# Kernel tuning notes

Hardware: AMD Instinct MI355X
Metric: run time of the kernel (lower is better)

## Reference

```python
import jax, jax.numpy as jnp
import numpy as np

N, T, D, E1 = 64, 32, 128, 128
EPS = 1e-6


def _mlp(x, W1, b1, W2, b2):
    # Linear -> ReLU -> (Dropout: identity in eval) -> Linear
    return jnp.maximum(x @ W1 + b1, 0.0) @ W2 + b2


def _forward(x_time, x_news,
             it_W1, it_b1, it_W2, it_b2,
             inw_W1, inw_b1, inw_W2, inw_b2,
             t2n_W1, t2n_b1, t2n_W2, t2n_b2,
             n2t_W1, n2t_b1, n2t_W2, n2t_b2,
             f_W1, f_b1, f_W2, f_b2,
             theta_t, theta_n):
    xt = x_time.reshape(-1, D)   # [NT, D]
    xn = x_news.reshape(-1, D)   # [NT, D]

    # incidence-matrix candidates, each [NT, E1]
    H_time = xt @ _mlp(xt.T, it_W1, it_b1, it_W2, it_b2)
    H_news = xn @ _mlp(xn.T, inw_W1, inw_b1, inw_W2, inw_b2)
    H_t2n = xt @ _mlp(xn.T, t2n_W1, t2n_b1, t2n_W2, t2n_b2)
    H_n2t = xn @ _mlp(xt.T, n2t_W1, n2t_b1, n2t_W2, n2t_b2)

    H = _mlp(jnp.concatenate([H_time, H_news, H_t2n, H_n2t], axis=1),
             f_W1, f_b1, f_W2, f_b2)  # [NT, E1]

    # column-wise standardization (torch.std is unbiased -> ddof=1) + softmax over nodes
    H = (H - H.mean(axis=0, keepdims=True)) / (H.std(axis=0, ddof=1, keepdims=True) + EPS)
    H = jax.nn.softmax(H, axis=0)

    # pairwise Jensen-Shannon divergence between columns of H -> [E1, E1]
    logH = jnp.log(H)
    M = (H[:, :, None] + H[:, None, :]) * 0.5          # [NT, E1, E1]
    kl_pm = jnp.sum(H[:, :, None] * (logH[:, :, None] - jnp.log(M)), axis=0)  # KL(P||M)
    # KL(Q||M)[i,j] == KL(P||M)[j,i] since M is symmetric in (i,j)
    jsd = (kl_pm + kl_pm.T) * 0.5

    jm = jsd.mean(axis=0)                               # [E1]
    njm = (jm - jm.mean()) / (jm.std(ddof=1) + EPS)
    w = jax.nn.softmax(njm)                             # diagonal of hyperedge weight W

    # Hypergraph conv with residual: x + elu(H @ diag(w) @ H.T @ x @ theta)
    # reassociated (exactly equal math) to avoid the O((NT)^2) intermediate
    Hw = H * w[None, :]                                 # [NT, E1]
    xt = xt + jax.nn.elu(Hw @ (H.T @ (xt @ theta_t)))
    xn = xn + jax.nn.elu(Hw @ (H.T @ (xn @ theta_n)))

    return xt.reshape(N, T, D), xn.reshape(N, T, D)


def setup_inputs() -> dict:
    key = jax.random.key(0)
    ks = iter(jax.random.split(key, 32))
    NT = N * T

    def lin(i, o):
        return (jax.random.normal(next(ks), (i, o), jnp.float32) / np.float32(np.sqrt(i)))

    inp = {
        "x_time": jax.random.normal(next(ks), (N, T, D), jnp.float32),
        "x_news": jax.random.normal(next(ks), (N, T, D), jnp.float32),
    }
    for pre in ["it", "inw", "t2n", "n2t"]:
        inp[pre + "_W1"] = lin(NT, E1)
        inp[pre + "_b1"] = jnp.zeros((E1,), jnp.float32)
        inp[pre + "_W2"] = lin(E1, E1)
        inp[pre + "_b2"] = jnp.zeros((E1,), jnp.float32)
    inp["f_W1"] = lin(4 * E1, E1)
    inp["f_b1"] = jnp.zeros((E1,), jnp.float32)
    inp["f_W2"] = lin(E1, E1)
    inp["f_b2"] = jnp.zeros((E1,), jnp.float32)
    # HypergraphConvolution uses torch.randn init for theta
    inp["theta_t"] = jax.random.normal(next(ks), (D, D), jnp.float32)
    inp["theta_n"] = jax.random.normal(next(ks), (D, D), jnp.float32)
    return inp


def reference(x_time, x_news,
              it_W1, it_b1, it_W2, it_b2,
              inw_W1, inw_b1, inw_W2, inw_b2,
              t2n_W1, t2n_b1, t2n_W2, t2n_b2,
              n2t_W1, n2t_b1, n2t_W2, n2t_b2,
              f_W1, f_b1, f_W2, f_b2,
              theta_t, theta_n):
    return _forward(x_time, x_news,
                    it_W1, it_b1, it_W2, it_b2,
                    inw_W1, inw_b1, inw_W2, inw_b2,
                    t2n_W1, t2n_b1, t2n_W2, t2n_b2,
                    n2t_W1, n2t_b1, n2t_W2, n2t_b2,
                    f_W1, f_b1, f_W2, f_b2,
                    theta_t, theta_n)
```

## Files before the change

### kernel.cpp

```cpp
#include <hip/hip_runtime.h>
#include <hip/hip_bf16.h>
#include <math.h>

#define NTOT 2048
#define DIM  128
#define MSPLIT 8
#define ZSPLIT 8
#define JT 16
#define JNC 128
#define JNSPLIT 8

struct P4 { const float* p[4]; };

__global__ __launch_bounds__(256) void gk_mlp1t(P4 X, P4 W1, float* __restrict__ Gs) {
  int k = blockIdx.z;
  int m0 = (blockIdx.x & 3) * 32;
  int e0 = (blockIdx.x >> 2) * 32;
  int split = blockIdx.y;
  int n0 = split * (NTOT / MSPLIT);
  const float* Xp = X.p[k];
  const float* Wp = W1.p[k];
  __shared__ float Xs[32][36], Ws[32][36];
  int tid = threadIdx.x;
  int lr = tid >> 3;
  int lc = (tid & 7) * 4;
  int tx = tid & 15, ty = tid >> 4;
  float a00 = 0.f, a01 = 0.f, a10 = 0.f, a11 = 0.f;
  for (int nb = 0; nb < NTOT / MSPLIT; nb += 32) {
    long gn = (long)(n0 + nb + lr) * DIM;
    float4 xv = *(const float4*)(Xp + gn + m0 + lc);
    float4 wv = *(const float4*)(Wp + gn + e0 + lc);
    *(float4*)&Xs[lr][lc] = xv;
    *(float4*)&Ws[lr][lc] = wv;
    __syncthreads();
    #pragma unroll
    for (int nn = 0; nn < 32; ++nn) {
      float x0 = Xs[nn][2*ty], x1 = Xs[nn][2*ty+1];
      float w0 = Ws[nn][2*tx], w1 = Ws[nn][2*tx+1];
      a00 += x0 * w0; a01 += x0 * w1;
      a10 += x1 * w0; a11 += x1 * w1;
    }
    __syncthreads();
  }
  float* Gk = Gs + ((long)k * MSPLIT + split) * 16384;
  int m = m0 + 2 * ty, e = e0 + 2 * tx;
  Gk[m * DIM + e]           = a00;
  Gk[m * DIM + e + 1]       = a01;
  Gk[(m + 1) * DIM + e]     = a10;
  Gk[(m + 1) * DIM + e + 1] = a11;
}

__global__ __launch_bounds__(128) void gk_mlp2(const float* __restrict__ Gs, P4 B1, P4 W2, P4 B2,
                                               float* __restrict__ M) {
  int m = blockIdx.x, e = threadIdx.x, k = blockIdx.y;
  __shared__ float a[DIM];
  const float* Gk = Gs + (long)k * MSPLIT * 16384 + m * DIM + e;
  float g = 0.f;
  #pragma unroll
  for (int s = 0; s < MSPLIT; ++s) g += Gk[s * 16384];
  a[e] = fmaxf(g + B1.p[k][e], 0.f);
  __syncthreads();
  const float* Wp = W2.p[k];
  float acc = B2.p[k][e];
  #pragma unroll 8
  for (int j = 0; j < DIM; ++j) acc += a[j] * Wp[(long)j * DIM + e];
  M[(long)k * 16384 + m * DIM + e] = acc;
}

__global__ __launch_bounds__(128) void gk_ab(const float* __restrict__ Mk, const float* __restrict__ fW1,
                                             float* __restrict__ AB) {
  int k = blockIdx.x, e = threadIdx.x, h = blockIdx.y;
  const float* Ma = Mk + (h == 0 ? 0 : 1) * 16384;
  const float* Mb = Mk + (h == 0 ? 2 : 3) * 16384;
  const float* W0 = fW1 + (h == 0 ? 0 : 128) * DIM;
  const float* W1p = fW1 + (h == 0 ? 256 : 384) * DIM;
  __shared__ float sa[DIM], sb[DIM];
  sa[e] = Ma[k * DIM + e];
  sb[e] = Mb[k * DIM + e];
  __syncthreads();
  float acc = 0.f;
  #pragma unroll 8
  for (int j = 0; j < DIM; ++j)
    acc += sa[j] * W0[(long)j * DIM + e] + sb[j] * W1p[(long)j * DIM + e];
  AB[(long)h * 16384 + k * DIM + e] = acc;
}

__global__ __launch_bounds__(128) void gk_h12(const float* __restrict__ xt, const float* __restrict__ xn,
                                              const float* __restrict__ AB, const float* __restrict__ fb1,
                                              const float* __restrict__ fW2, const float* __restrict__ fb2,
                                              float* __restrict__ Hraw) {
  int n = blockIdx.x, e = threadIdx.x;
  long xr = (long)n * DIM + e;
  __shared__ float st[DIM], sn[DIM], h1[DIM];
  st[e] = xt[xr];
  sn[e] = xn[xr];
  __syncthreads();
  float acc = 0.f;
  #pragma unroll 8
  for (int k = 0; k < DIM; ++k)
    acc += st[k] * AB[k * DIM + e] + sn[k] * AB[16384 + k * DIM + e];
  h1[e] = fmaxf(acc + fb1[e], 0.f);
  __syncthreads();
  float acc2 = fb2[e];
  #pragma unroll 8
  for (int j = 0; j < DIM; ++j) acc2 += h1[j] * fW2[(long)j * DIM + e];
  Hraw[(long)n * DIM + e] = acc2;
}

__global__ __launch_bounds__(256) void colsoft_k(const float* __restrict__ Hraw,
                                                 float* __restrict__ HTp, float* __restrict__ Ecol,
                                                 float* __restrict__ Gacc) {
  int e = blockIdx.x;
  int t = threadIdx.x;
  if (e == 0 && t < DIM) Gacc[t] = 0.f;
  __shared__ float sa[4], sb[4], sc[4];
  float v[8];
  float sum = 0.f, sq = 0.f, mx = -3.4e38f;
  #pragma unroll
  for (int r = 0; r < 8; ++r) {
    float x = Hraw[(long)(t + 256 * r) * DIM + e];
    v[r] = x;
    sum += x; sq += x * x; mx = fmaxf(mx, x);
  }
  #pragma unroll
  for (int o = 32; o > 0; o >>= 1) {
    sum += __shfl_down(sum, o);
    sq  += __shfl_down(sq, o);
    mx   = fmaxf(mx, __shfl_down(mx, o));
  }
  if ((t & 63) == 0) { int w = t >> 6; sa[w] = sum; sb[w] = sq; sc[w] = mx; }
  __syncthreads();
  sum = sa[0] + sa[1] + sa[2] + sa[3];
  sq  = sb[0] + sb[1] + sb[2] + sb[3];
  mx  = fmaxf(fmaxf(sc[0], sc[1]), fmaxf(sc[2], sc[3]));
  float mean = sum * (1.f / NTOT);
  float var  = (sq - sum * mean) * (1.f / (NTOT - 1));
  float ia   = 1.f / (sqrtf(fmaxf(var, 0.f)) + 1e-6f);
  float smax = (mx - mean) * ia;
  __syncthreads();

  float den = 0.f;
  #pragma unroll
  for (int r = 0; r < 8; ++r) {
    float s = (v[r] - mean) * ia - smax;
    v[r] = s;
    den += __expf(s);
  }
  #pragma unroll
  for (int o = 32; o > 0; o >>= 1) den += __shfl_down(den, o);
  if ((t & 63) == 0) sa[t >> 6] = den;
  __syncthreads();
  den = sa[0] + sa[1] + sa[2] + sa[3];
  float logden = __logf(den);
  float invden = 1.f / den;
  __syncthreads();

  float ent = 0.f;
  #pragma unroll
  for (int r = 0; r < 8; ++r) {
    float s = v[r];
    float pv = __expf(s) * invden;
    HTp[(long)e * NTOT + t + 256 * r] = pv;
    ent += pv * (s - logden);
  }
  #pragma unroll
  for (int o = 32; o > 0; o >>= 1) ent += __shfl_down(ent, o);
  if ((t & 63) == 0) sa[t >> 6] = ent;
  __syncthreads();
  if (t == 0) Ecol[e] = sa[0] + sa[1] + sa[2] + sa[3];
}

__global__ __launch_bounds__(256) void jsd_tile(const float* __restrict__ HTp,
                                                float* __restrict__ g) {
  int b = blockIdx.x;
  int bi = 0, rem = b;
  while (rem >= 8 - bi) { rem -= 8 - bi; ++bi; }
  int bj = bi + rem;
  int n0 = blockIdx.y * (NTOT / JNSPLIT);

  __shared__ float Ti[JT][JNC + 2];
  __shared__ float Tj[JT][JNC + 2];
  __shared__ float red[JT][JT + 1];

  int tid = threadIdx.x;
  int ti = tid >> 4, tj = tid & 15;
  bool active = (bi != bj) || (ti < tj);
  float acc = 0.f;

  int lc = tid >> 4;
  int ln = (tid & 15) * 8;

  for (int c = 0; c < NTOT / JNSPLIT; c += JNC) {
    const float* si = HTp + (long)(bi * JT + lc) * NTOT + n0 + c + ln;
    const float* sj = HTp + (long)(bj * JT + lc) * NTOT + n0 + c + ln;
    #pragma unroll
    for (int r = 0; r < 8; ++r) Ti[lc][ln + r] = si[r];
    #pragma unroll
    for (int r = 0; r < 8; ++r) Tj[lc][ln + r] = sj[r];
    __syncthreads();
    if (active) {
      #pragma unroll 4
      for (int n = 0; n < JNC; ++n) {
        float s = Ti[ti][n] + Tj[tj][n];
        acc += s * __logf(fmaxf(0.5f * s, 1e-38f));
      }
    }
    __syncthreads();
  }

  red[ti][tj] = active ? acc : 0.f;
  __syncthreads();
  if (tid < JT) {
    float s = 0.f;
    #pragma unroll
    for (int j = 0; j < JT; ++j) s += red[tid][j];
    atomicAdd(&g[bi * JT + tid], -s);
  } else if (tid < 2 * JT) {
    int c2 = tid - JT;
    float s = 0.f;
    #pragma unroll
    for (int i = 0; i < JT; ++i) s += red[i][c2];
    atomicAdd(&g[bj * JT + c2], -s);
  }
}

__global__ __launch_bounds__(128) void wvec_k(const float* __restrict__ g, const float* __restrict__ Ecol,
                                              float* __restrict__ w) {
  __shared__ float s2[2];
  int t = threadIdx.x;
  float e = Ecol[t];
  float v = e;
  #pragma unroll
  for (int o = 32; o > 0; o >>= 1) v += __shfl_down(v, o);
  if ((t & 63) == 0) s2[t >> 6] = v;
  __syncthreads();
  float S = s2[0] + s2[1];
  __syncthreads();
  float jm = (g[t] + 126.f * e + S) * (1.0f / 256.0f);
  v = jm;
  #pragma unroll
  for (int o = 32; o > 0; o >>= 1) v += __shfl_down(v, o);
  if ((t & 63) == 0) s2[t >> 6] = v;
  __syncthreads();
  float mean = (s2[0] + s2[1]) * (1.0f / 128.0f);
  __syncthreads();
  float d = jm - mean;
  v = d * d;
  #pragma unroll
  for (int o = 32; o > 0; o >>= 1) v += __shfl_down(v, o);
  if ((t & 63) == 0) s2[t >> 6] = v;
  __syncthreads();
  float var = (s2[0] + s2[1]) * (1.0f / 127.0f);
  float njm = d / (sqrtf(var) + 1e-6f);
  __syncthreads();
  v = njm;
  #pragma unroll
  for (int o = 32; o > 0; o >>= 1) v = fmaxf(v, __shfl_down(v, o));
  if ((t & 63) == 0) s2[t >> 6] = v;
  __syncthreads();
  float mx = fmaxf(s2[0], s2[1]);
  float ex = __expf(njm - mx);
  __syncthreads();
  v = ex;
  #pragma unroll
  for (int o = 32; o > 0; o >>= 1) v += __shfl_down(v, o);
  if ((t & 63) == 0) s2[t >> 6] = v;
  __syncthreads();
  w[t] = ex / (s2[0] + s2[1]);
}

__global__ __launch_bounds__(256) void xz_k(const float* __restrict__ HTp, const float* __restrict__ xt,
                                            const float* __restrict__ xn, float* __restrict__ Xzs) {
  int bt = blockIdx.z;
  const float* x = bt ? xn : xt;
  int split = blockIdx.y;
  float* C = Xzs + ((long)bt * ZSPLIT + split) * 16384;
  int e0 = (blockIdx.x & 3) * 32, d0 = (blockIdx.x >> 2) * 32;
  int n0 = split * (NTOT / ZSPLIT);
  __shared__ float As[32][33], Bs[32][36];
  int tid = threadIdx.x, col = tid & 31, row = tid >> 5;
  int lr = tid >> 3, lc4 = (tid & 7) * 4;
  int tx = tid & 15, ty = tid >> 4;
  float a00 = 0.f, a01 = 0.f, a10 = 0.f, a11 = 0.f;
  for (int nb = 0; nb < NTOT / ZSPLIT; nb += 32) {
    #pragma unroll
    for (int r = 0; r < 4; ++r) {
      int er = row + r * 8;
      As[col][er] = HTp[(long)(e0 + er) * NTOT + n0 + nb + col];
    }
    *(float4*)&Bs[lr][lc4] = *(const float4*)(x + (long)(n0 + nb + lr) * DIM + d0 + lc4);
    __syncthreads();
    #pragma unroll
    for (int nn = 0; nn < 32; ++nn) {
      float e0v = As[nn][2*ty], e1v = As[nn][2*ty+1];
      float d0v = Bs[nn][2*tx], d1v = Bs[nn][2*tx+1];
      a00 += e0v * d0v; a01 += e0v * d1v;
      a10 += e1v * d0v; a11 += e1v * d1v;
    }
    __syncthreads();
  }
  int e = e0 + 2 * ty, d = d0 + 2 * tx;
  C[e * DIM + d]           = a00;
  C[e * DIM + d + 1]       = a01;
  C[(e + 1) * DIM + d]     = a10;
  C[(e + 1) * DIM + d + 1] = a11;
}

__global__ __launch_bounds__(128) void zs_k(const float* __restrict__ Xzs, const float* __restrict__ thT,
                                            const float* __restrict__ thN, const float* __restrict__ w,
                                            float* __restrict__ Zw) {
  int e = blockIdx.x, d = threadIdx.x, bt = blockIdx.y;
  const float* src = Xzs + (long)bt * ZSPLIT * 16384 + e * DIM + d;
  const float* th = bt ? thN : thT;
  __shared__ float s[DIM];
  float xv = 0.f;
  #pragma unroll
  for (int sp = 0; sp < ZSPLIT; ++sp) xv += src[sp * 16384];
  s[d] = xv;
  __syncthreads();
  float acc = 0.f;
  #pragma unroll 8
  for (int k = 0; k < DIM; ++k) acc += s[k] * th[(long)k * DIM + d];
  Zw[bt * 16384 + e * DIM + d] = acc * w[e];
}

__global__ __launch_bounds__(256) void uk_t(const float* __restrict__ HTp, const float* __restrict__ Zw,
                                            const float* __restrict__ xt, const float* __restrict__ xn,
                                            float* __restrict__ out) {
  int bt = blockIdx.z;
  const float* x = bt ? xn : xt;
  const float* B = Zw + bt * 16384;
  float* o = out + (long)bt * NTOT * DIM;
  int d0 = blockIdx.x * 32, n0 = blockIdx.y * 32;
  __shared__ float As[32][33], Bs[32][36];
  int tid = threadIdx.x, col = tid & 31, row = tid >> 5;
  int lr = tid >> 3, lc4 = (tid & 7) * 4;
  int tx = tid & 15, ty = tid >> 4;
  float a00 = 0.f, a01 = 0.f, a10 = 0.f, a11 = 0.f;
  for (int eb = 0; eb < DIM; eb += 32) {
    #pragma unroll
    for (int r = 0; r < 4; ++r) {
      int rr = row + r * 8;
      As[col][rr] = HTp[(long)(eb + rr) * NTOT + n0 + col];
    }
    *(float4*)&Bs[lr][lc4] = *(const float4*)(B + (long)(eb + lr) * DIM + d0 + lc4);
    __syncthreads();
    #pragma unroll
    for (int ee = 0; ee < 32; ++ee) {
      float x0 = As[2*ty][ee], x1 = As[2*ty+1][ee];
      float b0 = Bs[ee][2*tx], b1 = Bs[ee][2*tx+1];
      a00 += x0 * b0; a01 += x0 * b1;
      a10 += x1 * b0; a11 += x1 * b1;
    }
    __syncthreads();
  }
  int n = n0 + 2 * ty, d = d0 + 2 * tx;
  long i0 = (long)n * DIM + d, i1 = i0 + DIM;
  float e00 = a00 > 0.f ? a00 : expm1f(a00);
  float e01 = a01 > 0.f ? a01 : expm1f(a01);
  float e10 = a10 > 0.f ? a10 : expm1f(a10);
  float e11 = a11 > 0.f ? a11 : expm1f(a11);
  o[i0]     = x[i0]     + e00;
  o[i0 + 1] = x[i0 + 1] + e01;
  o[i1]     = x[i1]     + e10;
  o[i1 + 1] = x[i1 + 1] + e11;
}

extern "C" void kernel_launch(void* const* d_in, const int* in_sizes, int n_in,
                              void* d_out, int out_size, void* d_ws, size_t ws_size,
                              hipStream_t stream) {
  const float* xt = (const float*)d_in[0];
  const float* xn = (const float*)d_in[1];
  const float *W1[4], *b1[4], *W2[4], *b2[4];
  for (int k = 0; k < 4; ++k) {
    W1[k] = (const float*)d_in[2 + 4*k];
    b1[k] = (const float*)d_in[3 + 4*k];
    W2[k] = (const float*)d_in[4 + 4*k];
    b2[k] = (const float*)d_in[5 + 4*k];
  }
  const float* fW1 = (const float*)d_in[18];
  const float* fb1 = (const float*)d_in[19];
  const float* fW2 = (const float*)d_in[20];
  const float* fb2 = (const float*)d_in[21];
  const float* thT = (const float*)d_in[22];
  const float* thN = (const float*)d_in[23];

  float* ws    = (float*)d_ws;
  float* Gacc  = ws;
  float* Ecol  = ws + 128;
  float* Wv    = ws + 256;
  float* Zw    = ws + 384;
  float* Xzs   = ws + 33152;
  float* Gs    = ws + 295296;
  float* Mk    = ws + 819584;
  float* AB    = ws + 885120;
  float* Hraw  = ws + 917888;
  float* HTp   = ws + 1180032;

  float* out = (float*)d_out;

  P4 Xs  = {{xt, xn, xn, xt}};
  P4 W1s = {{W1[0], W1[1], W1[2], W1[3]}};
  P4 B1s = {{b1[0], b1[1], b1[2], b1[3]}};
  P4 W2s = {{W2[0], W2[1], W2[2], W2[3]}};
  P4 B2s = {{b2[0], b2[1], b2[2], b2[3]}};

  gk_mlp1t<<<dim3(16, MSPLIT, 4), 256, 0, stream>>>(Xs, W1s, Gs);
  gk_mlp2<<<dim3(128, 4), 128, 0, stream>>>(Gs, B1s, W2s, B2s, Mk);
  gk_ab  <<<dim3(128, 2), 128, 0, stream>>>(Mk, fW1, AB);
  gk_h12 <<<NTOT, 128, 0, stream>>>(xt, xn, AB, fb1, fW2, fb2, Hraw);

  colsoft_k<<<DIM, 256, 0, stream>>>(Hraw, HTp, Ecol, Gacc);

  jsd_tile<<<dim3(36, JNSPLIT), 256, 0, stream>>>(HTp, Gacc);
  wvec_k<<<1, 128, 0, stream>>>(Gacc, Ecol, Wv);

  xz_k<<<dim3(16, ZSPLIT, 2), 256, 0, stream>>>(HTp, xt, xn, Xzs);
  zs_k<<<dim3(128, 2), 128, 0, stream>>>(Xzs, thT, thN, Wv, Zw);
  uk_t<<<dim3(4, 64, 2), 256, 0, stream>>>(HTp, Zw, xt, xn, out);

  (void)in_sizes; (void)n_in; (void)out_size; (void)ws_size;
}
```

Before: 191.7 us.

## Fuse MLP stages, batch H rows per block, prefetch GEMM tiles, inline weight vector

After: 183.8 us. -4.1%, faster.

```diff
diff --git a/kernel.cpp b/kernel.cpp
--- a/kernel.cpp
+++ b/kernel.cpp
@@ -26,13 +26,18 @@
   int lc = (tid & 7) * 4;
   int tx = tid & 15, ty = tid >> 4;
   float a00 = 0.f, a01 = 0.f, a10 = 0.f, a11 = 0.f;
+  long g0 = (long)(n0 + lr) * DIM;
+  float4 xv = *(const float4*)(Xp + g0 + m0 + lc);
+  float4 wv = *(const float4*)(Wp + g0 + e0 + lc);
   for (int nb = 0; nb < NTOT / MSPLIT; nb += 32) {
-    long gn = (long)(n0 + nb + lr) * DIM;
-    float4 xv = *(const float4*)(Xp + gn + m0 + lc);
-    float4 wv = *(const float4*)(Wp + gn + e0 + lc);
     *(float4*)&Xs[lr][lc] = xv;
     *(float4*)&Ws[lr][lc] = wv;
     __syncthreads();
+    if (nb + 32 < NTOT / MSPLIT) {
+      long gn = (long)(n0 + nb + 32 + lr) * DIM;
+      xv = *(const float4*)(Xp + gn + m0 + lc);
+      wv = *(const float4*)(Wp + gn + e0 + lc);
+    }
     #pragma unroll
     for (int nn = 0; nn < 32; ++nn) {
       float x0 = Xs[nn][2*ty], x1 = Xs[nn][2*ty+1];
@@ -50,64 +55,105 @@
   Gk[(m + 1) * DIM + e + 1] = a11;
 }
 
-__global__ __launch_bounds__(128) void gk_mlp2(const float* __restrict__ Gs, P4 B1, P4 W2, P4 B2,
-                                               float* __restrict__ M) {
-  int m = blockIdx.x, e = threadIdx.x, k = blockIdx.y;
-  __shared__ float a[DIM];
-  const float* Gk = Gs + (long)k * MSPLIT * 16384 + m * DIM + e;
-  float g = 0.f;
-  #pragma unroll
-  for (int s = 0; s < MSPLIT; ++s) g += Gk[s * 16384];
-  a[e] = fmaxf(g + B1.p[k][e], 0.f);
-  __syncthreads();
-  const float* Wp = W2.p[k];
-  float acc = B2.p[k][e];
-  #pragma unroll 8
-  for (int j = 0; j < DIM; ++j) acc += a[j] * Wp[(long)j * DIM + e];
-  M[(long)k * 16384 + m * DIM + e] = acc;
-}
-
-__global__ __launch_bounds__(128) void gk_ab(const float* __restrict__ Mk, const float* __restrict__ fW1,
-                                             float* __restrict__ AB) {
-  int k = blockIdx.x, e = threadIdx.x, h = blockIdx.y;
-  const float* Ma = Mk + (h == 0 ? 0 : 1) * 16384;
-  const float* Mb = Mk + (h == 0 ? 2 : 3) * 16384;
-  const float* W0 = fW1 + (h == 0 ? 0 : 128) * DIM;
-  const float* W1p = fW1 + (h == 0 ? 256 : 384) * DIM;
-  __shared__ float sa[DIM], sb[DIM];
-  sa[e] = Ma[k * DIM + e];
-  sb[e] = Mb[k * DIM + e];
-  __syncthreads();
+__global__ __launch_bounds__(256) void gk_mab(const float* __restrict__ Gs, P4 B1, P4 W2, P4 B2,
+                                              const float* __restrict__ fW1, float* __restrict__ AB) {
+  int m = blockIdx.x;
+  int e = threadIdx.x & 127;
+  int half = threadIdx.x >> 7;
+  int k0 = half, k1 = half + 2;
+  __shared__ float rk[4][DIM];
+  __shared__ float mk[4][DIM];
+  {
+    const float* G0 = Gs + (long)k0 * MSPLIT * 16384 + m * DIM + e;
+    const float* G1 = Gs + (long)k1 * MSPLIT * 16384 + m * DIM + e;
+    float s0 = 0.f, s1 = 0.f;
+    #pragma unroll
+    for (int s = 0; s < MSPLIT; ++s) { s0 += G0[s * 16384]; s1 += G1[s * 16384]; }
+    rk[k0][e] = fmaxf(s0 + B1.p[k0][e], 0.f);
+    rk[k1][e] = fmaxf(s1 + B1.p[k1][e], 0.f);
+  }
+  __syncthreads();
+  {
+    const float* Wa = W2.p[k0];
+    const float* Wb = W2.p[k1];
+    float a0 = B2.p[k0][e], a1 = B2.p[k1][e];
+    #pragma unroll 8
+    for (int j = 0; j < DIM; ++j) {
+      a0 += rk[k0][j] * Wa[j * DIM + e];
+      a1 += rk[k1][j] * Wb[j * DIM + e];
+    }
+    mk[k0][e] = a0;
+    mk[k1][e] = a1;
+  }
+  __syncthreads();
+  const float* Ma = mk[half];
+  const float* Mb = mk[half + 2];
+  const float* W0 = fW1 + (half == 0 ? 0 : 128) * DIM;
+  const float* W1p = fW1 + (half == 0 ? 256 : 384) * DIM;
   float acc = 0.f;
   #pragma unroll 8
   for (int j = 0; j < DIM; ++j)
-    acc += sa[j] * W0[(long)j * DIM + e] + sb[j] * W1p[(long)j * DIM + e];
-  AB[(long)h * 16384 + k * DIM + e] = acc;
-}
-
-__global__ __launch_bounds__(128) void gk_h12(const float* __restrict__ xt, const float* __restrict__ xn,
-                                              const float* __restrict__ AB, const float* __restrict__ fb1,
-                                              const float* __restrict__ fW2, const float* __restrict__ fb2,
-                                              float* __restrict__ Hraw) {
-  int n = blockIdx.x, e = threadIdx.x;
-  long xr = (long)n * DIM + e;
-  __shared__ float st[DIM], sn[DIM], h1[DIM];
-  st[e] = xt[xr];
-  sn[e] = xn[xr];
-  __syncthreads();
-  float acc = 0.f;
+    acc += Ma[j] * W0[j * DIM + e] + Mb[j] * W1p[j * DIM + e];
+  AB[(long)half * 16384 + m * DIM + e] = acc;
+}
+
+__global__ __launch_bounds__(256) void gk_h12t(const float* __restrict__ xt, const float* __restrict__ xn,
+                                               const float* __restrict__ AB, const float* __restrict__ fb1,
+                                               const float* __restrict__ fW2, const float* __restrict__ fb2,
+                                               float* __restrict__ HrawT) {
+  int n0 = blockIdx.x * 8;
+  int e  = threadIdx.x & 127;
+  int rr = (threadIdx.x >> 7) << 2;
+  __shared__ float stT[DIM][8], snT[DIM][8], h1T[DIM][8];
+  {
+    int c = threadIdx.x & 31, rq = threadIdx.x >> 5;
+    const float* xtr = xt + (long)(n0 + rq) * DIM;
+    const float* xnr = xn + (long)(n0 + rq) * DIM;
+    #pragma unroll
+    for (int i = 0; i < 4; ++i) {
+      int d = c + 32 * i;
+      stT[d][rq] = xtr[d];
+      snT[d][rq] = xnr[d];
+    }
+  }
+  __syncthreads();
+  float4 acc1 = make_float4(0.f, 0.f, 0.f, 0.f);
   #pragma unroll 8
-  for (int k = 0; k < DIM; ++k)
-    acc += st[k] * AB[k * DIM + e] + sn[k] * AB[16384 + k * DIM + e];
-  h1[e] = fmaxf(acc + fb1[e], 0.f);
-  __syncthreads();
-  float acc2 = fb2[e];
+  for (int k = 0; k < DIM; ++k) {
+    float a = AB[k * DIM + e];
+    float b = AB[16384 + k * DIM + e];
+    const float4 xv = *(const float4*)&stT[k][rr];
+    const float4 nv = *(const float4*)&snT[k][rr];
+    acc1.x += xv.x * a + nv.x * b;
+    acc1.y += xv.y * a + nv.y * b;
+    acc1.z += xv.z * a + nv.z * b;
+    acc1.w += xv.w * a + nv.w * b;
+  }
+  float b1v = fb1[e];
+  float4 h1;
+  h1.x = fmaxf(acc1.x + b1v, 0.f);
+  h1.y = fmaxf(acc1.y + b1v, 0.f);
+  h1.z = fmaxf(acc1.z + b1v, 0.f);
+  h1.w = fmaxf(acc1.w + b1v, 0.f);
+  *(float4*)&h1T[e][rr] = h1;
+  __syncthreads();
+  float4 acc2 = make_float4(0.f, 0.f, 0.f, 0.f);
   #pragma unroll 8
-  for (int j = 0; j < DIM; ++j) acc2 += h1[j] * fW2[(long)j * DIM + e];
-  Hraw[(long)n * DIM + e] = acc2;
-}
-
-__global__ __launch_bounds__(256) void colsoft_k(const float* __restrict__ Hraw,
+  for (int j = 0; j < DIM; ++j) {
+    float wv = fW2[j * DIM + e];
+    const float4 hv = *(const float4*)&h1T[j][rr];
+    acc2.x += hv.x * wv;
+    acc2.y += hv.y * wv;
+    acc2.z += hv.z * wv;
+    acc2.w += hv.w * wv;
+  }
+  float b2v = fb2[e];
+  float4 o;
+  o.x = acc2.x + b2v; o.y = acc2.y + b2v; o.z = acc2.z + b2v; o.w = acc2.w + b2v;
+  *(float4*)&HrawT[(long)e * NTOT + n0 + rr] = o;
+}
+
+__global__ __launch_bounds__(256) void colsoft_k(const float* __restrict__ HrawT,
                                                  float* __restrict__ HTp, float* __restrict__ Ecol,
                                                  float* __restrict__ Gacc) {
   int e = blockIdx.x;
@@ -118,7 +164,7 @@
   float sum = 0.f, sq = 0.f, mx = -3.4e38f;
   #pragma unroll
   for (int r = 0; r < 8; ++r) {
-    float x = Hraw[(long)(t + 256 * r) * DIM + e];
+    float x = HrawT[(long)e * NTOT + t + 256 * r];
     v[r] = x;
     sum += x; sq += x * x; mx = fmaxf(mx, x);
   }
@@ -222,51 +268,6 @@
     for (int i = 0; i < JT; ++i) s += red[i][c2];
     atomicAdd(&g[bj * JT + c2], -s);
   }
-}
-
-__global__ __launch_bounds__(128) void wvec_k(const float* __restrict__ g, const float* __restrict__ Ecol,
-                                              float* __restrict__ w) {
-  __shared__ float s2[2];
-  int t = threadIdx.x;
-  float e = Ecol[t];
-  float v = e;
-  #pragma unroll
-  for (int o = 32; o > 0; o >>= 1) v += __shfl_down(v, o);
-  if ((t & 63) == 0) s2[t >> 6] = v;
-  __syncthreads();
-  float S = s2[0] + s2[1];
-  __syncthreads();
-  float jm = (g[t] + 126.f * e + S) * (1.0f / 256.0f);
-  v = jm;
-  #pragma unroll
-  for (int o = 32; o > 0; o >>= 1) v += __shfl_down(v, o);
-  if ((t & 63) == 0) s2[t >> 6] = v;
-  __syncthreads();
-  float mean = (s2[0] + s2[1]) * (1.0f / 128.0f);
-  __syncthreads();
-  float d = jm - mean;
-  v = d * d;
-  #pragma unroll
-  for (int o = 32; o > 0; o >>= 1) v += __shfl_down(v, o);
-  if ((t & 63) == 0) s2[t >> 6] = v;
-  __syncthreads();
-  float var = (s2[0] + s2[1]) * (1.0f / 127.0f);
-  float njm = d / (sqrtf(var) + 1e-6f);
-  __syncthreads();
-  v = njm;
-  #pragma unroll
-  for (int o = 32; o > 0; o >>= 1) v = fmaxf(v, __shfl_down(v, o));
-  if ((t & 63) == 0) s2[t >> 6] = v;
-  __syncthreads();
-  float mx = fmaxf(s2[0], s2[1]);
-  float ex = __expf(njm - mx);
-  __syncthreads();
-  v = ex;
-  #pragma unroll
-  for (int o = 32; o > 0; o >>= 1) v += __shfl_down(v, o);
-  if ((t & 63) == 0) s2[t >> 6] = v;
-  __syncthreads();
-  w[t] = ex / (s2[0] + s2[1]);
 }
 
 __global__ __launch_bounds__(256) void xz_k(const float* __restrict__ HTp, const float* __restrict__ xt,
@@ -282,14 +283,21 @@
   int lr = tid >> 3, lc4 = (tid & 7) * 4;
   int tx = tid & 15, ty = tid >> 4;
   float a00 = 0.f, a01 = 0.f, a10 = 0.f, a11 = 0.f;
+  float pa[4]; float4 pb;
+  #pragma unroll
+  for (int r = 0; r < 4; ++r) pa[r] = HTp[(long)(e0 + row + r * 8) * NTOT + n0 + col];
+  pb = *(const float4*)(x + (long)(n0 + lr) * DIM + d0 + lc4);
   for (int nb = 0; nb < NTOT / ZSPLIT; nb += 32) {
     #pragma unroll
-    for (int r = 0; r < 4; ++r) {
-      int er = row + r * 8;
-      As[col][er] = HTp[(long)(e0 + er) * NTOT + n0 + nb + col];
-    }
-    *(float4*)&Bs[lr][lc4] = *(const float4*)(x + (long)(n0 + nb + lr) * DIM + d0 + lc4);
-    __syncthreads();
+    for (int r = 0; r < 4; ++r) As[col][row + r * 8] = pa[r];
+    *(float4*)&Bs[lr][lc4] = pb;
+    __syncthreads();
+    if (nb + 32 < NTOT / ZSPLIT) {
+      #pragma unroll
+      for (int r = 0; r < 4; ++r)
+        pa[r] = HTp[(long)(e0 + row + r * 8) * NTOT + n0 + nb + 32 + col];
+      pb = *(const float4*)(x + (long)(n0 + nb + 32 + lr) * DIM + d0 + lc4);
+    }
     #pragma unroll
     for (int nn = 0; nn < 32; ++nn) {
       float e0v = As[nn][2*ty], e1v = As[nn][2*ty+1];
@@ -307,9 +315,54 @@
 }
 
 __global__ __launch_bounds__(128) void zs_k(const float* __restrict__ Xzs, const float* __restrict__ thT,
-                                            const float* __restrict__ thN, const float* __restrict__ w,
-                                            float* __restrict__ Zw) {
+                                            const float* __restrict__ thN, const float* __restrict__ g,
+                                            const float* __restrict__ Ecol, float* __restrict__ Zw) {
   int e = blockIdx.x, d = threadIdx.x, bt = blockIdx.y;
+  __shared__ float s2[2];
+  __shared__ float swv;
+  int t = d;
+  float ec = Ecol[t];
+  float v = ec;
+  #pragma unroll
+  for (int o = 32; o > 0; o >>= 1) v += __shfl_down(v, o);
+  if ((t & 63) == 0) s2[t >> 6] = v;
+  __syncthreads();
+  float S = s2[0] + s2[1];
+  __syncthreads();
+  float jm = (g[t] + 126.f * ec + S) * (1.0f / 256.0f);
+  v = jm;
+  #pragma unroll
+  for (int o = 32; o > 0; o >>= 1) v += __shfl_down(v, o);
+  if ((t & 63) == 0) s2[t >> 6] = v;
+  __syncthreads();
+  float mean = (s2[0] + s2[1]) * (1.0f / 128.0f);
+  __syncthreads();
+  float dv = jm - mean;
+  v = dv * dv;
+  #pragma unroll
+  for (int o = 32; o > 0; o >>= 1) v += __shfl_down(v, o);
+  if ((t & 63) == 0) s2[t >> 6] = v;
+  __syncthreads();
+  float var = (s2[0] + s2[1]) * (1.0f / 127.0f);
+  float njm = dv / (sqrtf(var) + 1e-6f);
+  __syncthreads();
+  v = njm;
+  #pragma unroll
+  for (int o = 32; o > 0; o >>= 1) v = fmaxf(v, __shfl_down(v, o));
+  if ((t & 63) == 0) s2[t >> 6] = v;
+  __syncthreads();
+  float mx = fmaxf(s2[0], s2[1]);
+  float ex = __expf(njm - mx);
+  __syncthreads();
+  v = ex;
+  #pragma unroll
+  for (int o = 32; o > 0; o >>= 1) v += __shfl_down(v, o);
+  if ((t & 63) == 0) s2[t >> 6] = v;
+  __syncthreads();
+  if (t == e) swv = ex / (s2[0] + s2[1]);
+  __syncthreads();
+  float we = swv;
+
   const float* src = Xzs + (long)bt * ZSPLIT * 16384 + e * DIM + d;
   const float* th = bt ? thN : thT;
   __shared__ float s[DIM];
@@ -321,7 +374,7 @@
   float acc = 0.f;
   #pragma unroll 8
   for (int k = 0; k < DIM; ++k) acc += s[k] * th[(long)k * DIM + d];
-  Zw[bt * 16384 + e * DIM + d] = acc * w[e];
+  Zw[bt * 16384 + e * DIM + d] = acc * we;
 }
 
 __global__ __launch_bounds__(256) void uk_t(const float* __restrict__ HTp, const float* __restrict__ Zw,
@@ -337,14 +390,21 @@
   int lr = tid >> 3, lc4 = (tid & 7) * 4;
   int tx = tid & 15, ty = tid >> 4;
   float a00 = 0.f, a01 = 0.f, a10 = 0.f, a11 = 0.f;
+  float pa[4]; float4 pb;
+  #pragma unroll
+  for (int r = 0; r < 4; ++r) pa[r] = HTp[(long)(row + r * 8) * NTOT + n0 + col];
+  pb = *(const float4*)(B + (long)lr * DIM + d0 + lc4);
   for (int eb = 0; eb < DIM; eb += 32) {
     #pragma unroll
-    for (int r = 0; r < 4; ++r) {
-      int rr = row + r * 8;
-      As[col][rr] = HTp[(long)(eb + rr) * NTOT + n0 + col];
-    }
-    *(float4*)&Bs[lr][lc4] = *(const float4*)(B + (long)(eb + lr) * DIM + d0 + lc4);
-    __syncthreads();
+    for (int r = 0; r < 4; ++r) As[col][row + r * 8] = pa[r];
+    *(float4*)&Bs[lr][lc4] = pb;
+    __syncthreads();
+    if (eb + 32 < DIM) {
+      #pragma unroll
+      for (int r = 0; r < 4; ++r)
+        pa[r] = HTp[(long)(eb + 32 + row + r * 8) * NTOT + n0 + col];
+      pb = *(const float4*)(B + (long)(eb + 32 + lr) * DIM + d0 + lc4);
+    }
     #pragma unroll
     for (int ee = 0; ee < 32; ++ee) {
       float x0 = As[2*ty][ee], x1 = As[2*ty+1][ee];
@@ -388,13 +448,11 @@
   float* ws    = (float*)d_ws;
   float* Gacc  = ws;
   float* Ecol  = ws + 128;
-  float* Wv    = ws + 256;
   float* Zw    = ws + 384;
   float* Xzs   = ws + 33152;
   float* Gs    = ws + 295296;
-  float* Mk    = ws + 819584;
   float* AB    = ws + 885120;
-  float* Hraw  = ws + 917888;
+  float* HrawT = ws + 917888;
   float* HTp   = ws + 1180032;
 
   float* out = (float*)d_out;
@@ -406,17 +464,15 @@
   P4 B2s = {{b2[0], b2[1], b2[2], b2[3]}};
 
   gk_mlp1t<<<dim3(16, MSPLIT, 4), 256, 0, stream>>>(Xs, W1s, Gs);
-  gk_mlp2<<<dim3(128, 4), 128, 0, stream>>>(Gs, B1s, W2s, B2s, Mk);
-  gk_ab  <<<dim3(128, 2), 128, 0, stream>>>(Mk, fW1, AB);
-  gk_h12 <<<NTOT, 128, 0, stream>>>(xt, xn, AB, fb1, fW2, fb2, Hraw);
-
-  colsoft_k<<<DIM, 256, 0, stream>>>(Hraw, HTp, Ecol, Gacc);
+  gk_mab  <<<128, 256, 0, stream>>>(Gs, B1s, W2s, B2s, fW1, AB);
+  gk_h12t <<<256, 256, 0, stream>>>(xt, xn, AB, fb1, fW2, fb2, HrawT);
+
+  colsoft_k<<<DIM, 256, 0, stream>>>(HrawT, HTp, Ecol, Gacc);
 
   jsd_tile<<<dim3(36, JNSPLIT), 256, 0, stream>>>(HTp, Gacc);
-  wvec_k<<<1, 128, 0, stream>>>(Gacc, Ecol, Wv);
 
   xz_k<<<dim3(16, ZSPLIT, 2), 256, 0, stream>>>(HTp, xt, xn, Xzs);
-  zs_k<<<dim3(128, 2), 128, 0, stream>>>(Xzs, thT, thN, Wv, Zw);
+  zs_k<<<dim3(128, 2), 128, 0, stream>>>(Xzs, thT, thN, Gacc, Ecol, Zw);
   uk_t<<<dim3(4, 64, 2), 256, 0, stream>>>(HTp, Zw, xt, xn, out);
 
   (void)in_sizes; (void)n_in; (void)out_size; (void)ws_size;
```
